# Kernel optimization log

Measured on AMD Instinct MI355X. Metric: run time of the kernel, lower is better.

Reference implementation:

```python
import jax, jax.numpy as jnp
import numpy as np

B, T, C, H = 2, 2048, 1024, 16
HS = C // H  # 64
FF = 4 * C
EPS = 1e-5


def _ln(x, g, b):
    mu = jnp.mean(x, axis=-1, keepdims=True)
    var = jnp.var(x, axis=-1, keepdims=True)
    return (x - mu) * jax.lax.rsqrt(var + EPS) * g + b


def setup_inputs() -> dict:
    key = jax.random.key(0)
    ks = jax.random.split(key, 16)
    s = 0.02
    return {
        'x':  jax.random.normal(ks[0], (B, T, C), jnp.float32),
        # per-head q/k/v weights stacked: [H, C, HS], biases [H, HS]
        'Wq': jax.random.normal(ks[1], (H, C, HS), jnp.float32) * s,
        'bq': jax.random.normal(ks[2], (H, HS), jnp.float32) * s,
        'Wk': jax.random.normal(ks[3], (H, C, HS), jnp.float32) * s,
        'bk': jax.random.normal(ks[4], (H, HS), jnp.float32) * s,
        'Wv': jax.random.normal(ks[5], (H, C, HS), jnp.float32) * s,
        'bv': jax.random.normal(ks[6], (H, HS), jnp.float32) * s,
        'Wp': jax.random.normal(ks[7], (C, C), jnp.float32) * s,
        'bp': jax.random.normal(ks[8], (C,), jnp.float32) * s,
        'W1': jax.random.normal(ks[9], (C, FF), jnp.float32) * s,
        'b1': jax.random.normal(ks[10], (FF,), jnp.float32) * s,
        'W2': jax.random.normal(ks[11], (FF, C), jnp.float32) * s,
        'b2': jax.random.normal(ks[12], (C,), jnp.float32) * s,
        'g1': 1.0 + jax.random.normal(ks[13], (C,), jnp.float32) * s,
        'be1': jax.random.normal(ks[14], (C,), jnp.float32) * s,
        'g2': 1.0 + jax.random.normal(ks[15], (C,), jnp.float32) * s,
        'be2': jnp.zeros((C,), jnp.float32),
    }


def reference(x, Wq, bq, Wk, bk, Wv, bv, Wp, bp, W1, b1, W2, b2, g1, be1, g2, be2):
    # Multi-head causal self-attention (non-residual block, eval mode: dropout = identity)
    q = jnp.einsum('btc,hcd->bhtd', x, Wq) + bq[None, :, None, :]
    k = jnp.einsum('btc,hcd->bhtd', x, Wk) + bk[None, :, None, :]
    v = jnp.einsum('btc,hcd->bhtd', x, Wv) + bv[None, :, None, :]
    scores = jnp.einsum('bhtd,bhsd->bhts', q, k) * (HS ** -0.5)
    causal = jnp.tril(jnp.ones((T, T), bool))
    scores = jnp.where(causal, scores, -jnp.inf)
    wei = jax.nn.softmax(scores, axis=-1)
    out = jnp.einsum('bhts,bhsd->bhtd', wei, v)       # [B,H,T,HS]
    out = out.transpose(0, 2, 1, 3).reshape(B, T, C)  # concat heads
    h = out @ Wp + bp
    h = _ln(h, g1, be1)
    # FeedForward: Linear -> ReLU -> Linear -> ReLU -> Dropout(eval=id)
    f = jax.nn.relu(h @ W1 + b1)
    f = jax.nn.relu(f @ W2 + b2)
    return _ln(f, g2, be2)
```

## Files before the change

### kernel.cpp

```cpp
#include <hip/hip_runtime.h>

typedef __bf16 bf16x8 __attribute__((ext_vector_type(8)));
typedef float f32x4 __attribute__((ext_vector_type(4)));
typedef unsigned int u32x4 __attribute__((ext_vector_type(4)));

__device__ __forceinline__ float b2f(ushort h) {
  union { unsigned u; float f; } x; x.u = ((unsigned)h) << 16; return x.f;
}
__device__ __forceinline__ ushort f2b(float f) {
  union { float f; unsigned u; } x; x.f = f;
  unsigned r = x.u + 0x7fffu + ((x.u >> 16) & 1u);
  return (ushort)(r >> 16);
}
__device__ __forceinline__ ushort f2b_trunc(float f) {
  union { float f; unsigned u; } x; x.f = f;
  return (ushort)(x.u >> 16);
}
static ushort f2b_host(float f) {
  union { float f; unsigned u; } x; x.f = f;
  unsigned r = x.u + 0x7fffu + ((x.u >> 16) & 1u);
  return (ushort)(r >> 16);
}
__device__ __forceinline__ float ldp(const void* p, int i, int f32) {
  return f32 ? ((const float*)p)[i] : b2f(((const ushort*)p)[i]);
}

typedef const __attribute__((address_space(1))) unsigned int* gas_p;
typedef __attribute__((address_space(3))) unsigned int* las_p;
__device__ __forceinline__ void cp16(const ushort* g, ushort* l) {
  __builtin_amdgcn_global_load_lds((gas_p)g, (las_p)l, 16, 0, 0);
}

__global__ __launch_bounds__(256) void fill_sentinel(ushort* out, ushort v) {
  out[(size_t)blockIdx.x * 256 + threadIdx.x] = v;
}

__global__ void sniff_dtype(const ushort* __restrict__ x, int* __restrict__ flag) {
  int ln = threadIdx.x;
  int hit = 0;
#pragma unroll
  for (int i = 0; i < 64; ++i) {
    ushort v = x[ln * 64 + i];
    int e = (v >> 7) & 0xff;
    hit |= (e >= 200) ? 1 : 0;
  }
  unsigned long long b = __ballot(hit);
  if (ln == 0) *flag = (b != 0ull) ? 1 : 0;
}

__global__ __launch_bounds__(256) void convert_x(
    const void* __restrict__ src, ushort* __restrict__ dst, const int* __restrict__ flagp) {
  int f32 = *flagp;
  size_t i = ((size_t)blockIdx.x * 256 + threadIdx.x) * 8;
  if (f32) {
    const float* s = (const float*)src;
    ushort4 o0, o1;
    o0.x = f2b(s[i + 0]); o0.y = f2b(s[i + 1]); o0.z = f2b(s[i + 2]); o0.w = f2b(s[i + 3]);
    o1.x = f2b(s[i + 4]); o1.y = f2b(s[i + 5]); o1.z = f2b(s[i + 6]); o1.w = f2b(s[i + 7]);
    *(ushort4*)(dst + i) = o0;
    *(ushort4*)(dst + i + 4) = o1;
  } else {
    *(u32x4*)(dst + i) = *(const u32x4*)((const ushort*)src + i);
  }
}

__global__ __launch_bounds__(256) void transpose_w(
    const void* __restrict__ src, ushort* __restrict__ dst,
    int R, int Ccols, long sb, long db, const int* __restrict__ flagp) {
  int f32 = *flagp;
  __shared__ ushort tile[32][33];
  int bz = blockIdx.z;
  const float* sf = (const float*)src + (long)bz * sb;
  const ushort* su = (const ushort*)src + (long)bz * sb;
  dst += (long)bz * db;
  int c0 = blockIdx.x * 32, r0 = blockIdx.y * 32;
  int x = threadIdx.x, y = threadIdx.y;
#pragma unroll
  for (int i = 0; i < 32; i += 8) {
    long idx = (long)(r0 + y + i) * Ccols + (c0 + x);
    tile[y + i][x] = f32 ? f2b(sf[idx]) : su[idx];
  }
  __syncthreads();
#pragma unroll
  for (int i = 0; i < 32; i += 8)
    dst[(long)(c0 + y + i) * R + (r0 + x)] = tile[x][y + i];
}

__global__ __launch_bounds__(256) void transpose_bf16(
    const ushort* __restrict__ src, ushort* __restrict__ dst,
    int R, int Ccols, long sb, long db) {
  __shared__ ushort tile[32][33];
  int bz = blockIdx.z;
  src += (long)bz * sb; dst += (long)bz * db;
  int c0 = blockIdx.x * 32, r0 = blockIdx.y * 32;
  int x = threadIdx.x, y = threadIdx.y;
#pragma unroll
  for (int i = 0; i < 32; i += 8)
    tile[y + i][x] = src[(long)(r0 + y + i) * Ccols + (c0 + x)];
  __syncthreads();
#pragma unroll
  for (int i = 0; i < 32; i += 8)
    dst[(long)(c0 + y + i) * R + (r0 + x)] = tile[x][y + i];
}

#define GSTR 32
template <int MODE>
__global__ __launch_bounds__(256, 4) void gemm_bt(
    const ushort* __restrict__ A, const ushort* __restrict__ Bt,
    const void* __restrict__ bias0, const void* __restrict__ bias1,
    const void* __restrict__ bias2, ushort* __restrict__ C,
    ushort* __restrict__ Qo, ushort* __restrict__ Ko, ushort* __restrict__ Vo,
    int M, int N, int K, const int* __restrict__ flagp) {
  int f32 = *flagp;
  __shared__ __align__(16) ushort ldsA[128 * GSTR];
  __shared__ __align__(16) ushort ldsB[128 * GSTR];
  int tid = threadIdx.x;
  int wv = tid >> 6, ln = tid & 63;
  int lane15 = ln & 15, quad = ln >> 4;
  int nb = blockIdx.x * 128, mb = blockIdx.y * 128;
  int wr = (wv & 1) * 64, wc = (wv >> 1) * 64;
  f32x4 acc[4][4] = {};
  const ushort* Abase = A + (size_t)mb * K;
  const ushort* Bbase = Bt + (size_t)nb * K;
  int arow = tid >> 2, acol = (tid & 3) * 8;

  for (int kk = 0; kk < K; kk += 32) {
    __syncthreads();
#pragma unroll
    for (int c = 0; c < 2; ++c) {
      cp16(Abase + (size_t)(c * 64 + arow) * K + kk + acol, &ldsA[c * 2048 + tid * 8]);
      cp16(Bbase + (size_t)(c * 64 + arow) * K + kk + acol, &ldsB[c * 2048 + tid * 8]);
    }
    __syncthreads();
    bf16x8 af[4], bfr[4];
#pragma unroll
    for (int t = 0; t < 4; ++t) {
      af[t] = *(const bf16x8*)&ldsA[(wr + t * 16 + lane15) * GSTR + quad * 8];
      bfr[t] = *(const bf16x8*)&ldsB[(wc + t * 16 + lane15) * GSTR + quad * 8];
    }
#pragma unroll
    for (int mt = 0; mt < 4; ++mt)
#pragma unroll
      for (int nt = 0; nt < 4; ++nt)
        acc[mt][nt] = __builtin_amdgcn_mfma_f32_16x16x32_bf16(af[mt], bfr[nt], acc[mt][nt], 0, 0, 0);
  }

#pragma unroll
  for (int nt = 0; nt < 4; ++nt) {
    int col = nb + wc + nt * 16 + lane15;
    float bvv;
    if constexpr (MODE == 2) {
      int which = col >> 10;
      const void* bs = (which == 0) ? bias0 : (which == 1) ? bias1 : bias2;
      bvv = ldp(bs, col & 1023, f32);
    } else {
      bvv = ldp(bias0, col, f32);
    }
#pragma unroll
    for (int mt = 0; mt < 4; ++mt) {
#pragma unroll
      for (int r = 0; r < 4; ++r) {
        int row = mb + wr + mt * 16 + quad * 4 + r;
        float val = acc[mt][nt][r] + bvv;
        if constexpr (MODE == 1) val = fmaxf(val, 0.0f);
        if constexpr (MODE == 2) {
          int which = col >> 10, hh = (col >> 6) & 15, d = col & 63;
          int bb = row >> 11, t = row & 2047;
          size_t idx = (((size_t)bb * 16 + hh) * 2048 + t) * 64 + d;
          ushort o = f2b(val);
          if (which == 0) Qo[idx] = o;
          else if (which == 1) Ko[idx] = o;
          else Vo[idx] = o;
        } else {
          C[(size_t)row * N + col] = f2b(val);
        }
      }
    }
  }
}

template <int MODE>
__global__ __launch_bounds__(256, 4) void gemm_bt64(
    const ushort* __restrict__ A, const ushort* __restrict__ Bt,
    const void* __restrict__ bias0, ushort* __restrict__ C,
    int M, int N, int K, const int* __restrict__ flagp) {
  int f32 = *flagp;
  __shared__ __align__(16) ushort ldsA[128 * 32];
  __shared__ __align__(16) ushort ldsB[64 * 32];
  int tid = threadIdx.x;
  int wv = tid >> 6, ln = tid & 63;
  int lane15 = ln & 15, quad = ln >> 4;
  int nb = blockIdx.x * 64, mb = blockIdx.y * 128;
  int wr = wv * 32;
  f32x4 acc[2][4] = {};
  const ushort* Abase = A + (size_t)mb * K;
  const ushort* Bbase = Bt + (size_t)nb * K;
  int arow = tid >> 2, acol = (tid & 3) * 8;

  for (int kk = 0; kk < K; kk += 32) {
    __syncthreads();
#pragma unroll
    for (int c = 0; c < 2; ++c)
      cp16(Abase + (size_t)(c * 64 + arow) * K + kk + acol, &ldsA[c * 2048 + tid * 8]);
    cp16(Bbase + (size_t)arow * K + kk + acol, &ldsB[tid * 8]);
    __syncthreads();
    bf16x8 af[2], bfr[4];
#pragma unroll
    for (int t = 0; t < 2; ++t)
      af[t] = *(const bf16x8*)&ldsA[(wr + t * 16 + lane15) * 32 + quad * 8];
#pragma unroll
    for (int t = 0; t < 4; ++t)
      bfr[t] = *(const bf16x8*)&ldsB[(t * 16 + lane15) * 32 + quad * 8];
#pragma unroll
    for (int mt = 0; mt < 2; ++mt)
#pragma unroll
      for (int nt = 0; nt < 4; ++nt)
        acc[mt][nt] = __builtin_amdgcn_mfma_f32_16x16x32_bf16(af[mt], bfr[nt], acc[mt][nt], 0, 0, 0);
  }

#pragma unroll
  for (int nt = 0; nt < 4; ++nt) {
    int col = nb + nt * 16 + lane15;
    float bvv = ldp(bias0, col, f32);
#pragma unroll
    for (int mt = 0; mt < 2; ++mt) {
#pragma unroll
      for (int r = 0; r < 4; ++r) {
        int row = mb + wr + mt * 16 + quad * 4 + r;
        float val = acc[mt][nt][r] + bvv;
        if constexpr (MODE == 1) val = fmaxf(val, 0.0f);
        C[(size_t)row * N + col] = f2b(val);
      }
    }
  }
}

#define ASTR 68
__global__ __launch_bounds__(256) void attn_kernel(
    const ushort* __restrict__ q, const ushort* __restrict__ k,
    const ushort* __restrict__ vT, ushort* __restrict__ out) {
  __shared__ __align__(16) ushort ldsK[64 * ASTR];
  __shared__ __align__(16) ushort ldsV[64 * ASTR];
  __shared__ __align__(16) ushort ldsP[4][16 * ASTR];
  int qt = (gridDim.x - 1) - blockIdx.x;
  int bh = blockIdx.y;
  int b = bh >> 4, h = bh & 15;
  int tid = threadIdx.x, wv = tid >> 6, ln = tid & 63;
  int lane15 = ln & 15, quad = ln >> 4;
  size_t bhT = (size_t)bh * 2048;
  int qbase = qt * 64;
  int qrl = wv * 16;

  bf16x8 qf[2];
  {
    const ushort* qp = q + (bhT + qbase + qrl + lane15) * 64 + quad * 8;
    qf[0] = *(const bf16x8*)qp;
    qf[1] = *(const bf16x8*)(qp + 32);
    const float qscale = 0.125f * 1.44269504f;
#pragma unroll
    for (int i = 0; i < 8; ++i) {
      qf[0][i] = (__bf16)((float)qf[0][i] * qscale);
      qf[1][i] = (__bf16)((float)qf[1][i] * qscale);
    }
  }
  bf16x8 onesf;
#pragma unroll
  for (int i = 0; i < 8; ++i) onesf[i] = (__bf16)1.0f;

  f32x4 o[4] = {};
  f32x4 lsum = {};
  int srow = tid >> 3, scol = (tid & 7) * 8;

  for (int kb = 0; kb <= qt; ++kb) {
    int kbase = kb * 64;
    __syncthreads();
#pragma unroll
    for (int c = 0; c < 2; ++c) {
      int row = c * 32 + srow;
      u32x4 kvv = *(const u32x4*)(k + (bhT + kbase + row) * 64 + scol);
      u32x4 vvv = *(const u32x4*)(vT + ((size_t)bh * 64 + row) * 2048 + kbase + scol);
      *(u32x4*)&ldsK[row * ASTR + scol] = kvv;
      *(u32x4*)&ldsV[row * ASTR + scol] = vvv;
    }
    __syncthreads();

    f32x4 s[4];
#pragma unroll
    for (int nt = 0; nt < 4; ++nt) {
      f32x4 a = {};
#pragma unroll
      for (int ks = 0; ks < 2; ++ks) {
        bf16x8 bf = *(const bf16x8*)&ldsK[(nt * 16 + lane15) * ASTR + ks * 32 + quad * 8];
        a = __builtin_amdgcn_mfma_f32_16x16x32_bf16(qf[ks], bf, a, 0, 0, 0);
      }
      s[nt] = a;
    }
    if (kb == qt) {
#pragma unroll
      for (int nt = 0; nt < 4; ++nt)
#pragma unroll
        for (int r = 0; r < 4; ++r) {
          int qrow = qrl + quad * 4 + r;
          int kcol = nt * 16 + lane15;
          float p = (kcol > qrow) ? 0.0f : __builtin_amdgcn_exp2f(s[nt][r]);
          ldsP[wv][(quad * 4 + r) * ASTR + nt * 16 + lane15] = f2b_trunc(p);
        }
    } else {
#pragma unroll
      for (int nt = 0; nt < 4; ++nt)
#pragma unroll
        for (int r = 0; r < 4; ++r)
          ldsP[wv][(quad * 4 + r) * ASTR + nt * 16 + lane15] =
              f2b_trunc(__builtin_amdgcn_exp2f(s[nt][r]));
    }
    bf16x8 pa[2];
    pa[0] = *(const bf16x8*)&ldsP[wv][lane15 * ASTR + quad * 8];
    pa[1] = *(const bf16x8*)&ldsP[wv][lane15 * ASTR + 32 + quad * 8];
#pragma unroll
    for (int ks = 0; ks < 2; ++ks)
      lsum = __builtin_amdgcn_mfma_f32_16x16x32_bf16(pa[ks], onesf, lsum, 0, 0, 0);
#pragma unroll
    for (int dt = 0; dt < 4; ++dt)
#pragma unroll
      for (int ks = 0; ks < 2; ++ks) {
        bf16x8 vb = *(const bf16x8*)&ldsV[(dt * 16 + lane15) * ASTR + ks * 32 + quad * 8];
        o[dt] = __builtin_amdgcn_mfma_f32_16x16x32_bf16(pa[ks], vb, o[dt], 0, 0, 0);
      }
  }

#pragma unroll
  for (int dt = 0; dt < 4; ++dt)
#pragma unroll
    for (int r = 0; r < 4; ++r) {
      int qrow = qbase + qrl + quad * 4 + r;
      float val = o[dt][r] / lsum[r];
      out[((size_t)b * 2048 + qrow) * 1024 + h * 64 + dt * 16 + lane15] = f2b(val);
    }
}

template <int FINAL>
__global__ __launch_bounds__(256) void ln_kernel(
    const ushort* x, const void* g, const void* be, void* outv,
    const int* __restrict__ flagp) {
  int f32 = *flagp;
  int row = blockIdx.x;
  const ushort* xr = x + (size_t)row * 1024;
  int tid = threadIdx.x;
  ushort4 hv = ((const ushort4*)xr)[tid];
  float v0 = b2f(hv.x), v1 = b2f(hv.y), v2 = b2f(hv.z), v3 = b2f(hv.w);
  float s = v0 + v1 + v2 + v3;
  float s2 = v0 * v0 + v1 * v1 + v2 * v2 + v3 * v3;
#pragma unroll
  for (int off = 1; off < 64; off <<= 1) {
    s += __shfl_xor(s, off);
    s2 += __shfl_xor(s2, off);
  }
  __shared__ float red[8];
  int wv = tid >> 6;
  if ((tid & 63) == 0) { red[wv] = s; red[4 + wv] = s2; }
  __syncthreads();
  s = red[0] + red[1] + red[2] + red[3];
  s2 = red[4] + red[5] + red[6] + red[7];
  float mean = s * (1.f / 1024.f);
  float var = s2 * (1.f / 1024.f) - mean * mean;
  float rstd = rsqrtf(var + 1e-5f);
  int c = tid * 4;
  float r0 = (v0 - mean) * rstd * ldp(g, c + 0, f32) + ldp(be, c + 0, f32);
  float r1 = (v1 - mean) * rstd * ldp(g, c + 1, f32) + ldp(be, c + 1, f32);
  float r2 = (v2 - mean) * rstd * ldp(g, c + 2, f32) + ldp(be, c + 2, f32);
  float r3 = (v3 - mean) * rstd * ldp(g, c + 3, f32) + ldp(be, c + 3, f32);
  if (FINAL && f32) {
    float4 ov = make_float4(r0, r1, r2, r3);
    ((float4*)((float*)outv + (size_t)row * 1024))[tid] = ov;
  } else {
    ushort4 ov;
    ov.x = f2b(r0); ov.y = f2b(r1); ov.z = f2b(r2); ov.w = f2b(r3);
    ((ushort4*)((ushort*)outv + (size_t)row * 1024))[tid] = ov;
  }
}

extern "C" void kernel_launch(void* const* d_in, const int* in_sizes, int n_in,
                              void* d_out, int out_size, void* d_ws, size_t ws_size,
                              hipStream_t stream) {
  ushort* dout = (ushort*)d_out;
  bool ok_sizes = (n_in == 17) && out_size == 4194304 &&
                  in_sizes[0] == 4194304 && in_sizes[1] == 1048576 && in_sizes[2] == 1024 &&
                  in_sizes[3] == 1048576 && in_sizes[5] == 1048576 && in_sizes[7] == 1048576 &&
                  in_sizes[8] == 1024 && in_sizes[9] == 4194304 && in_sizes[10] == 4096 &&
                  in_sizes[11] == 4194304 && in_sizes[13] == 1024;
  if (!ok_sizes) {
    fill_sentinel<<<dim3(16384), dim3(256), 0, stream>>>(dout, f2b_host(774144.f));
    return;
  }
  const size_t NEED = 58720260;
  if (ws_size < NEED) {
    fill_sentinel<<<dim3(16384), dim3(256), 0, stream>>>(
        dout, f2b_host(1000.f + (float)(ws_size >> 20)));
    return;
  }

  const void* x   = d_in[0];
  const void* Wq  = d_in[1];
  const void* bq  = d_in[2];
  const void* Wk  = d_in[3];
  const void* bk  = d_in[4];
  const void* Wv  = d_in[5];
  const void* bv  = d_in[6];
  const void* Wp  = d_in[7];
  const void* bp  = d_in[8];
  const void* W1  = d_in[9];
  const void* b1  = d_in[10];
  const void* W2  = d_in[11];
  const void* b2  = d_in[12];
  const void* g1  = d_in[13];
  const void* be1 = d_in[14];
  const void* g2  = d_in[15];
  const void* be2 = d_in[16];

  ushort* ws    = (ushort*)d_ws;
  ushort* xb    = ws;
  ushort* bt2   = ws;
  ushort* btqkv = ws + 4194304;
  ushort* btp   = ws + 7340032;
  ushort* bt1   = ws + 8388608;
  ushort* qb    = ws + 12582912;
  ushort* kbuf  = ws + 16777216;
  ushort* vbuf  = ws + 20971520;
  ushort* vt    = ws + 25165824;
  ushort* f1    = ws + 12582912;
  ushort* f2    = ws + 4194304;
  int*    flagp = (int*)((char*)d_ws + 58720256);
  ushort* attn  = dout;
  ushort* hproj = qb;
  ushort* hln   = dout;

  dim3 blk(256);
  dim3 tb(32, 8);
  sniff_dtype<<<dim3(1), dim3(64), 0, stream>>>((const ushort*)x, flagp);
  convert_x<<<dim3(2048), blk, 0, stream>>>(x, xb, flagp);
  transpose_w<<<dim3(2, 32, 16), tb, 0, stream>>>(Wq, btqkv, 1024, 64, 65536, 65536, flagp);
  transpose_w<<<dim3(2, 32, 16), tb, 0, stream>>>(Wk, btqkv + 1048576, 1024, 64, 65536, 65536, flagp);
  transpose_w<<<dim3(2, 32, 16), tb, 0, stream>>>(Wv, btqkv + 2097152, 1024, 64, 65536, 65536, flagp);
  transpose_w<<<dim3(32, 32, 1), tb, 0, stream>>>(Wp, btp, 1024, 1024, 0, 0, flagp);
  transpose_w<<<dim3(128, 32, 1), tb, 0, stream>>>(W1, bt1, 1024, 4096, 0, 0, flagp);
  gemm_bt<2><<<dim3(24, 32), blk, 0, stream>>>(xb, btqkv, bq, bk, bv, nullptr, qb, kbuf, vbuf,
                                               4096, 3072, 1024, flagp);
  transpose_w<<<dim3(32, 128, 1), tb, 0, stream>>>(W2, bt2, 4096, 1024, 0, 0, flagp);
  transpose_bf16<<<dim3(2, 64, 32), tb, 0, stream>>>(vbuf, vt, 2048, 64, 131072, 131072);
  attn_kernel<<<dim3(32, 32), blk, 0, stream>>>(qb, kbuf, vt, attn);
  gemm_bt64<0><<<dim3(16, 32), blk, 0, stream>>>(attn, btp, bp, hproj, 4096, 1024, 1024, flagp);
  ln_kernel<0><<<dim3(4096), blk, 0, stream>>>(hproj, g1, be1, hln, flagp);
  gemm_bt<1><<<dim3(32, 32), blk, 0, stream>>>(hln, bt1, b1, nullptr, nullptr, f1,
                                               nullptr, nullptr, nullptr, 4096, 4096, 1024, flagp);
  gemm_bt64<1><<<dim3(16, 32), blk, 0, stream>>>(f1, bt2, b2, f2, 4096, 1024, 4096, flagp);
  ln_kernel<1><<<dim3(4096), blk, 0, stream>>>(f2, g2, be2, d_out, flagp);
}
```

Measured before the change: 424.2 us.

## Load K/V MFMA fragments directly from global memory, dropping LDS staging and barriers

```diff
diff --git a/kernel.cpp b/kernel.cpp
--- a/kernel.cpp
+++ b/kernel.cpp
@@ -236,11 +236,9 @@
 }
 
 #define ASTR 68
-__global__ __launch_bounds__(256) void attn_kernel(
+__global__ __launch_bounds__(256, 4) void attn_kernel(
     const ushort* __restrict__ q, const ushort* __restrict__ k,
     const ushort* __restrict__ vT, ushort* __restrict__ out) {
-  __shared__ __align__(16) ushort ldsK[64 * ASTR];
-  __shared__ __align__(16) ushort ldsV[64 * ASTR];
   __shared__ __align__(16) ushort ldsP[4][16 * ASTR];
   int qt = (gridDim.x - 1) - blockIdx.x;
   int bh = blockIdx.y;
@@ -267,33 +265,22 @@
 #pragma unroll
   for (int i = 0; i < 8; ++i) onesf[i] = (__bf16)1.0f;
 
+  const ushort* kp = k + (bhT + lane15) * 64 + quad * 8;
+  const ushort* vp = vT + ((size_t)bh * 64 + lane15) * 2048 + quad * 8;
+
   f32x4 o[4] = {};
   f32x4 lsum = {};
-  int srow = tid >> 3, scol = (tid & 7) * 8;
 
   for (int kb = 0; kb <= qt; ++kb) {
     int kbase = kb * 64;
-    __syncthreads();
-#pragma unroll
-    for (int c = 0; c < 2; ++c) {
-      int row = c * 32 + srow;
-      u32x4 kvv = *(const u32x4*)(k + (bhT + kbase + row) * 64 + scol);
-      u32x4 vvv = *(const u32x4*)(vT + ((size_t)bh * 64 + row) * 2048 + kbase + scol);
-      *(u32x4*)&ldsK[row * ASTR + scol] = kvv;
-      *(u32x4*)&ldsV[row * ASTR + scol] = vvv;
-    }
-    __syncthreads();
-
     f32x4 s[4];
 #pragma unroll
     for (int nt = 0; nt < 4; ++nt) {
-      f32x4 a = {};
-#pragma unroll
-      for (int ks = 0; ks < 2; ++ks) {
-        bf16x8 bf = *(const bf16x8*)&ldsK[(nt * 16 + lane15) * ASTR + ks * 32 + quad * 8];
-        a = __builtin_amdgcn_mfma_f32_16x16x32_bf16(qf[ks], bf, a, 0, 0, 0);
-      }
-      s[nt] = a;
+      const ushort* kr = kp + (size_t)(kbase + nt * 16) * 64;
+      bf16x8 bf0 = *(const bf16x8*)kr;
+      bf16x8 bf1 = *(const bf16x8*)(kr + 32);
+      f32x4 a = __builtin_amdgcn_mfma_f32_16x16x32_bf16(qf[0], bf0, f32x4{}, 0, 0, 0);
+      s[nt] = __builtin_amdgcn_mfma_f32_16x16x32_bf16(qf[1], bf1, a, 0, 0, 0);
     }
     if (kb == qt) {
 #pragma unroll
@@ -316,16 +303,16 @@
     bf16x8 pa[2];
     pa[0] = *(const bf16x8*)&ldsP[wv][lane15 * ASTR + quad * 8];
     pa[1] = *(const bf16x8*)&ldsP[wv][lane15 * ASTR + 32 + quad * 8];
-#pragma unroll
-    for (int ks = 0; ks < 2; ++ks)
-      lsum = __builtin_amdgcn_mfma_f32_16x16x32_bf16(pa[ks], onesf, lsum, 0, 0, 0);
-#pragma unroll
-    for (int dt = 0; dt < 4; ++dt)
-#pragma unroll
-      for (int ks = 0; ks < 2; ++ks) {
-        bf16x8 vb = *(const bf16x8*)&ldsV[(dt * 16 + lane15) * ASTR + ks * 32 + quad * 8];
-        o[dt] = __builtin_amdgcn_mfma_f32_16x16x32_bf16(pa[ks], vb, o[dt], 0, 0, 0);
-      }
+    lsum = __builtin_amdgcn_mfma_f32_16x16x32_bf16(pa[0], onesf, lsum, 0, 0, 0);
+    lsum = __builtin_amdgcn_mfma_f32_16x16x32_bf16(pa[1], onesf, lsum, 0, 0, 0);
+#pragma unroll
+    for (int dt = 0; dt < 4; ++dt) {
+      const ushort* vr = vp + (size_t)dt * 16 * 2048 + kbase;
+      bf16x8 vb0 = *(const bf16x8*)vr;
+      bf16x8 vb1 = *(const bf16x8*)(vr + 32);
+      o[dt] = __builtin_amdgcn_mfma_f32_16x16x32_bf16(pa[0], vb0, o[dt], 0, 0, 0);
+      o[dt] = __builtin_amdgcn_mfma_f32_16x16x32_bf16(pa[1], vb1, o[dt], 0, 0, 0);
+    }
   }
 
 #pragma unroll
```

After: 576.1 us. +35.8%, slower.

## Process two 64-row query tiles per attention block to reuse K/V loads

Applied to the files above, without the earlier changes.

```diff
diff --git a/kernel.cpp b/kernel.cpp
--- a/kernel.cpp
+++ b/kernel.cpp
@@ -236,42 +236,46 @@
 }
 
 #define ASTR 68
-__global__ __launch_bounds__(256) void attn_kernel(
+__global__ __launch_bounds__(256, 4) void attn_kernel(
     const ushort* __restrict__ q, const ushort* __restrict__ k,
     const ushort* __restrict__ vT, ushort* __restrict__ out) {
   __shared__ __align__(16) ushort ldsK[64 * ASTR];
   __shared__ __align__(16) ushort ldsV[64 * ASTR];
-  __shared__ __align__(16) ushort ldsP[4][16 * ASTR];
-  int qt = (gridDim.x - 1) - blockIdx.x;
+  __shared__ __align__(16) ushort ldsP[4][32 * ASTR];
+  int qi = (gridDim.x - 1) - blockIdx.x;
   int bh = blockIdx.y;
   int b = bh >> 4, h = bh & 15;
   int tid = threadIdx.x, wv = tid >> 6, ln = tid & 63;
   int lane15 = ln & 15, quad = ln >> 4;
   size_t bhT = (size_t)bh * 2048;
-  int qbase = qt * 64;
+  int qbase = qi * 128;
   int qrl = wv * 16;
-
-  bf16x8 qf[2];
+  int kmax = (qbase + 127) >> 6;
+
+  bf16x8 qf[2][2];
   {
-    const ushort* qp = q + (bhT + qbase + qrl + lane15) * 64 + quad * 8;
-    qf[0] = *(const bf16x8*)qp;
-    qf[1] = *(const bf16x8*)(qp + 32);
     const float qscale = 0.125f * 1.44269504f;
 #pragma unroll
-    for (int i = 0; i < 8; ++i) {
-      qf[0][i] = (__bf16)((float)qf[0][i] * qscale);
-      qf[1][i] = (__bf16)((float)qf[1][i] * qscale);
+    for (int m = 0; m < 2; ++m) {
+      const ushort* qp = q + (bhT + qbase + m * 64 + qrl + lane15) * 64 + quad * 8;
+      qf[m][0] = *(const bf16x8*)qp;
+      qf[m][1] = *(const bf16x8*)(qp + 32);
+#pragma unroll
+      for (int i = 0; i < 8; ++i) {
+        qf[m][0][i] = (__bf16)((float)qf[m][0][i] * qscale);
+        qf[m][1][i] = (__bf16)((float)qf[m][1][i] * qscale);
+      }
     }
   }
   bf16x8 onesf;
 #pragma unroll
   for (int i = 0; i < 8; ++i) onesf[i] = (__bf16)1.0f;
 
-  f32x4 o[4] = {};
-  f32x4 lsum = {};
+  f32x4 o[2][4] = {};
+  f32x4 lsum[2] = {};
   int srow = tid >> 3, scol = (tid & 7) * 8;
 
-  for (int kb = 0; kb <= qt; ++kb) {
+  for (int kb = 0; kb <= kmax; ++kb) {
     int kbase = kb * 64;
     __syncthreads();
 #pragma unroll
@@ -284,58 +288,63 @@
     }
     __syncthreads();
 
-    f32x4 s[4];
-#pragma unroll
-    for (int nt = 0; nt < 4; ++nt) {
-      f32x4 a = {};
-#pragma unroll
-      for (int ks = 0; ks < 2; ++ks) {
-        bf16x8 bf = *(const bf16x8*)&ldsK[(nt * 16 + lane15) * ASTR + ks * 32 + quad * 8];
-        a = __builtin_amdgcn_mfma_f32_16x16x32_bf16(qf[ks], bf, a, 0, 0, 0);
-      }
-      s[nt] = a;
-    }
-    if (kb == qt) {
-#pragma unroll
-      for (int nt = 0; nt < 4; ++nt)
-#pragma unroll
-        for (int r = 0; r < 4; ++r) {
-          int qrow = qrl + quad * 4 + r;
-          int kcol = nt * 16 + lane15;
-          float p = (kcol > qrow) ? 0.0f : __builtin_amdgcn_exp2f(s[nt][r]);
-          ldsP[wv][(quad * 4 + r) * ASTR + nt * 16 + lane15] = f2b_trunc(p);
+#pragma unroll
+    for (int m = 0; m < 2; ++m) {
+      int rowbase = qbase + m * 64 + qrl;
+      f32x4 s[4];
+#pragma unroll
+      for (int nt = 0; nt < 4; ++nt) {
+        f32x4 a = {};
+#pragma unroll
+        for (int ks = 0; ks < 2; ++ks) {
+          bf16x8 bf = *(const bf16x8*)&ldsK[(nt * 16 + lane15) * ASTR + ks * 32 + quad * 8];
+          a = __builtin_amdgcn_mfma_f32_16x16x32_bf16(qf[m][ks], bf, a, 0, 0, 0);
         }
-    } else {
-#pragma unroll
-      for (int nt = 0; nt < 4; ++nt)
-#pragma unroll
-        for (int r = 0; r < 4; ++r)
-          ldsP[wv][(quad * 4 + r) * ASTR + nt * 16 + lane15] =
-              f2b_trunc(__builtin_amdgcn_exp2f(s[nt][r]));
-    }
-    bf16x8 pa[2];
-    pa[0] = *(const bf16x8*)&ldsP[wv][lane15 * ASTR + quad * 8];
-    pa[1] = *(const bf16x8*)&ldsP[wv][lane15 * ASTR + 32 + quad * 8];
-#pragma unroll
-    for (int ks = 0; ks < 2; ++ks)
-      lsum = __builtin_amdgcn_mfma_f32_16x16x32_bf16(pa[ks], onesf, lsum, 0, 0, 0);
+        s[nt] = a;
+      }
+      if (kbase + 63 > rowbase) {
+#pragma unroll
+        for (int nt = 0; nt < 4; ++nt)
+#pragma unroll
+          for (int r = 0; r < 4; ++r) {
+            int qrow = rowbase + quad * 4 + r;
+            int kcol = kbase + nt * 16 + lane15;
+            float p = (kcol > qrow) ? 0.0f : __builtin_amdgcn_exp2f(s[nt][r]);
+            ldsP[wv][(m * 16 + quad * 4 + r) * ASTR + nt * 16 + lane15] = f2b_trunc(p);
+          }
+      } else {
+#pragma unroll
+        for (int nt = 0; nt < 4; ++nt)
+#pragma unroll
+          for (int r = 0; r < 4; ++r)
+            ldsP[wv][(m * 16 + quad * 4 + r) * ASTR + nt * 16 + lane15] =
+                f2b_trunc(__builtin_amdgcn_exp2f(s[nt][r]));
+      }
+      bf16x8 pa[2];
+      pa[0] = *(const bf16x8*)&ldsP[wv][(m * 16 + lane15) * ASTR + quad * 8];
+      pa[1] = *(const bf16x8*)&ldsP[wv][(m * 16 + lane15) * ASTR + 32 + quad * 8];
+      lsum[m] = __builtin_amdgcn_mfma_f32_16x16x32_bf16(pa[0], onesf, lsum[m], 0, 0, 0);
+      lsum[m] = __builtin_amdgcn_mfma_f32_16x16x32_bf16(pa[1], onesf, lsum[m], 0, 0, 0);
+#pragma unroll
+      for (int dt = 0; dt < 4; ++dt) {
+        bf16x8 vb0 = *(const bf16x8*)&ldsV[(dt * 16 + lane15) * ASTR + quad * 8];
+        bf16x8 vb1 = *(const bf16x8*)&ldsV[(dt * 16 + lane15) * ASTR + 32 + quad * 8];
+        o[m][dt] = __builtin_amdgcn_mfma_f32_16x16x32_bf16(pa[0], vb0, o[m][dt], 0, 0, 0);
+        o[m][dt] = __builtin_amdgcn_mfma_f32_16x16x32_bf16(pa[1], vb1, o[m][dt], 0, 0, 0);
+      }
+    }
+  }
+
+#pragma unroll
+  for (int m = 0; m < 2; ++m)
 #pragma unroll
     for (int dt = 0; dt < 4; ++dt)
 #pragma unroll
-      for (int ks = 0; ks < 2; ++ks) {
-        bf16x8 vb = *(const bf16x8*)&ldsV[(dt * 16 + lane15) * ASTR + ks * 32 + quad * 8];
-        o[dt] = __builtin_amdgcn_mfma_f32_16x16x32_bf16(pa[ks], vb, o[dt], 0, 0, 0);
-      }
-  }
-
-#pragma unroll
-  for (int dt = 0; dt < 4; ++dt)
-#pragma unroll
-    for (int r = 0; r < 4; ++r) {
-      int qrow = qbase + qrl + quad * 4 + r;
-      float val = o[dt][r] / lsum[r];
-      out[((size_t)b * 2048 + qrow) * 1024 + h * 64 + dt * 16 + lane15] = f2b(val);
-    }
+      for (int r = 0; r < 4; ++r) {
+        int qrow = qbase + m * 64 + qrl + quad * 4 + r;
+        float val = o[m][dt][r] / lsum[m][r];
+        out[((size_t)b * 2048 + qrow) * 1024 + h * 64 + dt * 16 + lane15] = f2b(val);
+      }
 }
 
 template <int FINAL>
@@ -447,7 +456,7 @@
                                                4096, 3072, 1024, flagp);
   transpose_w<<<dim3(32, 128, 1), tb, 0, stream>>>(W2, bt2, 4096, 1024, 0, 0, flagp);
   transpose_bf16<<<dim3(2, 64, 32), tb, 0, stream>>>(vbuf, vt, 2048, 64, 131072, 131072);
-  attn_kernel<<<dim3(32, 32), blk, 0, stream>>>(qb, kbuf, vt, attn);
+  attn_kernel<<<dim3(16, 32), blk, 0, stream>>>(qb, kbuf, vt, attn);
   gemm_bt64<0><<<dim3(16, 32), blk, 0, stream>>>(attn, btp, bp, hproj, 4096, 1024, 1024, flagp);
   ln_kernel<0><<<dim3(4096), blk, 0, stream>>>(hproj, g1, be1, hln, flagp);
   gemm_bt<1><<<dim3(32, 32), blk, 0, stream>>>(hln, bt1, b1, nullptr, nullptr, f1,
```

Measured after the change: 513.8 us. +21.1%, slower.
